# Kernel optimization log

Measured on AMD Instinct MI355X. Metric: run time of the kernel, lower is better.

## Reference

```python
import jax, jax.numpy as jnp
import numpy as np

PROCESSING_SPEED = 8.0  # init kwarg: softmax temperature
EPS = 1e-8              # torch F.cosine_similarity eps
BATCH, SIZE, DIM = 1024, 65536, 512


def setup_inputs() -> dict:
    key = jax.random.key(0)
    k1, k2 = jax.random.split(key)
    x = jax.random.normal(k1, (BATCH, DIM), dtype=jnp.float32)
    memory_bank = jax.random.normal(k2, (SIZE, DIM), dtype=jnp.float32)
    return {"x": x, "memory_bank": memory_bank}


def reference(x, memory_bank):
    # Cosine similarity between every query and every memory row, computed as
    # normalized dot products (math-equivalent to F.cosine_similarity with
    # denominator clamp max(||a||*||b||, eps), avoiding the (B,S,D) broadcast).
    x_norm = jnp.linalg.norm(x, axis=1, keepdims=True)            # (B, 1)
    m_norm = jnp.linalg.norm(memory_bank, axis=1, keepdims=True)  # (S, 1)
    dots = jnp.einsum('bd,sd->bs', x, memory_bank)                # (B, S)
    sims = dots / jnp.maximum(x_norm * m_norm.T, EPS)             # (B, S)
    attention = jax.nn.softmax(sims * PROCESSING_SPEED, axis=1)   # (B, S)
    return attention @ memory_bank                                # (B, D)
```

## Files before the change

kernel.cpp:

```cpp
#include <hip/hip_runtime.h>
#include <hip/hip_bf16.h>
#include <stdint.h>

#define B_N 1024
#define S_N 65536
#define D_N 512
#define NS 32
#define SC (S_N / NS)
#define SB 256
#define NSUB (SC / SB)

typedef __attribute__((ext_vector_type(8))) short bf16x8;
typedef __attribute__((ext_vector_type(4))) float f32x4;
typedef __attribute__((ext_vector_type(16))) float f32x16;

#define OFF_MBF   ((size_t)0)
#define OFF_MT    (OFF_MBF + (size_t)S_N * D_N * 2)
#define OFF_XBF   (OFF_MT  + (size_t)D_N * S_N * 2)
#define OFF_RX    (OFF_XBF + (size_t)B_N * D_N * 2)
#define OFF_RM    (OFF_RX  + (size_t)B_N * 4)
#define OFF_LSUM  (OFF_RM  + (size_t)S_N * 4)
#define OFF_OPART (OFF_LSUM + (size_t)B_N * 4)

__device__ __forceinline__ unsigned short f2bf(float f) {
  unsigned u = __builtin_bit_cast(unsigned, f);
  u += 0x7fffu + ((u >> 16) & 1u);
  return (unsigned short)(u >> 16);
}

__device__ __forceinline__ void stage16(const unsigned short* g, unsigned short* l) {
  __builtin_amdgcn_global_load_lds(
      (const __attribute__((address_space(1))) void*)g,
      (__attribute__((address_space(3))) void*)l, 16, 0, 0);
}

__global__ void k_prep_x(const float* __restrict__ X, unsigned short* __restrict__ Xbf,
                         float* __restrict__ rx) {
  const int row = blockIdx.x;
  const int t = threadIdx.x;
  float4 v = ((const float4*)(X + (size_t)row * D_N))[t];
  float ss = v.x*v.x + v.y*v.y + v.z*v.z + v.w*v.w;
  ushort4 o; o.x = f2bf(v.x); o.y = f2bf(v.y); o.z = f2bf(v.z); o.w = f2bf(v.w);
  ((ushort4*)(Xbf + (size_t)row * D_N))[t] = o;
  #pragma unroll
  for (int m = 1; m < 64; m <<= 1) ss += __shfl_xor(ss, m);
  __shared__ float partial[2];
  if ((t & 63) == 0) partial[t >> 6] = ss;
  __syncthreads();
  if (t == 0) rx[row] = 11.541560327111707f * rsqrtf(fmaxf(partial[0] + partial[1], 1e-24f));
}

__global__ void k_prep_m(const float* __restrict__ M, unsigned short* __restrict__ Mbf,
                         unsigned short* __restrict__ Mt, float* __restrict__ rm) {
  __shared__ float ts[64 * 65];
  const int t = threadIdx.x;
  const int s0 = blockIdx.x * 64;
  const int r = t >> 2, cq = t & 3;
  const int c = t >> 2, sq = t & 3;
  float ss = 0.f;
  for (int ct = 0; ct < 8; ++ct) {
    float f[16];
    const float4* src = (const float4*)(M + (size_t)(s0 + r) * D_N + ct * 64 + cq * 16);
    #pragma unroll
    for (int k = 0; k < 4; ++k) {
      float4 v = src[k];
      f[4*k+0] = v.x; f[4*k+1] = v.y; f[4*k+2] = v.z; f[4*k+3] = v.w;
    }
    union { unsigned short u[16]; uint4 v4[2]; } pk;
    #pragma unroll
    for (int j = 0; j < 16; ++j) {
      ss += f[j] * f[j];
      pk.u[j] = f2bf(f[j]);
      ts[r * 65 + cq * 16 + j] = f[j];
    }
    uint4* dst = (uint4*)(Mbf + (size_t)(s0 + r) * D_N + ct * 64 + cq * 16);
    dst[0] = pk.v4[0]; dst[1] = pk.v4[1];
    __syncthreads();
    union { unsigned short u[16]; uint4 v4[2]; } pt;
    #pragma unroll
    for (int j = 0; j < 16; ++j) pt.u[j] = f2bf(ts[(sq * 16 + j) * 65 + c]);
    uint4* dt = (uint4*)(Mt + (size_t)(ct * 64 + c) * S_N + s0 + sq * 16);
    dt[0] = pt.v4[0]; dt[1] = pt.v4[1];
    __syncthreads();
  }
  ss += __shfl_xor(ss, 1);
  ss += __shfl_xor(ss, 2);
  if (cq == 0) rm[s0 + r] = rsqrtf(fmaxf(ss, 1e-24f));
}

__global__ __launch_bounds__(512, 2) void k_fused(
    const unsigned short* __restrict__ Xbf, const unsigned short* __restrict__ Mbf,
    const unsigned short* __restrict__ Mt, const float* __restrict__ rx,
    const float* __restrict__ rminv, float* __restrict__ lsum,
    float* __restrict__ Opart) {
  __shared__ unsigned short Stg[2][24576];
  __shared__ unsigned short Ps[32768];

  const int t = threadIdx.x;
  const int w = t >> 6, lane = t & 63, l31 = lane & 31, hi = lane >> 5;
  const int qs = w >> 1, qcb = w & 1;
  const int hb = w >> 2, qd = w & 3;
  const int r7 = (l31 >> 1) & 7;
  const int p7 = l31 & 7;
  const int t3 = l31 & 3;
  const int sub8 = (lane & 1) * 8;
  const int rp15 = l31 >> 1;

  const int bid = blockIdx.x;
  const int xcd = bid & 7, slot = bid >> 3;
  const int bblk = slot & 7;
  const int chunk = xcd * 4 + (slot >> 3);
  const int b0 = bblk * 128;
  const int s0 = chunk * SC;

  const int mrow_t = ((t >> 4) << 1) | (t & 1);
  const int mc8    = ((((t >> 1) & 7) ^ ((t >> 4) & 7)) << 3);
  const int trow_t = t >> 2;
  const int tc8    = (((t & 3) ^ ((t >> 2) & 3)) << 3);

  #define ISS_QK(sS_, k0_, bi_) do {                                           \
    _Pragma("unroll")                                                          \
    for (int is = 0; is < 4; ++is)                                             \
      stage16(Mbf + (size_t)((sS_) + is * 64 + mrow_t) * D_N + (k0_) + mc8,    \
              &Stg[bi_][is * 4096 + w * 512]);                                 \
    _Pragma("unroll")                                                          \
    for (int is = 0; is < 2; ++is)                                             \
      stage16(Xbf + (size_t)(b0 + is * 64 + mrow_t) * D_N + (k0_) + mc8,       \
              &Stg[bi_][16384 + is * 4096 + w * 512]);                         \
  } while (0)
  #define ISS_T(sS_, ph_, bi_) do {                                            \
    _Pragma("unroll")                                                          \
    for (int is = 0; is < 4; ++is)                                             \
      stage16(Mt + (size_t)(is * 128 + trow_t) * S_N + (sS_) + (ph_) * 32 + tc8, \
              &Stg[bi_][is * 4096 + w * 512]);                                 \
  } while (0)

  f32x16 accO[2][4];
  #pragma unroll
  for (int i = 0; i < 2; ++i)
    #pragma unroll
    for (int j = 0; j < 4; ++j)
      #pragma unroll
      for (int r = 0; r < 16; ++r) accO[i][j][r] = 0.f;

  float ls[2] = {0.f, 0.f};
  float rxj[2];
  #pragma unroll
  for (int j = 0; j < 2; ++j) rxj[j] = rx[b0 + qcb * 64 + j * 32 + l31];

  ISS_QK(s0, 0, 0);

  for (int sub = 0; sub < NSUB; ++sub) {
    const int sS = s0 + sub * SB;

    f32x16 accP[2][2];
    #pragma unroll
    for (int i = 0; i < 2; ++i)
      #pragma unroll
      for (int j = 0; j < 2; ++j)
        #pragma unroll
        for (int r = 0; r < 16; ++r) accP[i][j][r] = 0.f;

    #pragma unroll
    for (int ph = 0; ph < 8; ++ph) {
      const int bi = ph & 1;
      if (ph < 7) { ISS_QK(sS, (ph + 1) * 64, bi ^ 1); }
      else        { ISS_T(sS, 0, bi ^ 1); }
      if (ph < 7) asm volatile("s_waitcnt vmcnt(6)" ::: "memory");
      else        asm volatile("s_waitcnt vmcnt(4)" ::: "memory");
      __builtin_amdgcn_s_barrier();
      const unsigned short* Ms = &Stg[bi][0];
      const unsigned short* Xs = &Stg[bi][16384];
      __builtin_amdgcn_s_setprio(1);
      #pragma unroll
      for (int ks = 0; ks < 4; ++ks) {
        const int c = ks * 2 + hi;
        bf16x8 aB[2], xB[2];
        #pragma unroll
        for (int i = 0; i < 2; ++i)
          aB[i] = *(const bf16x8*)&Ms[(qs * 32 + i * 16 + rp15) * 128 + ((c ^ r7) << 4) + sub8];
        #pragma unroll
        for (int j = 0; j < 2; ++j)
          xB[j] = *(const bf16x8*)&Xs[(qcb * 32 + j * 16 + rp15) * 128 + ((c ^ r7) << 4) + sub8];
        #pragma unroll
        for (int i = 0; i < 2; ++i)
          #pragma unroll
          for (int j = 0; j < 2; ++j)
            accP[i][j] = __builtin_amdgcn_mfma_f32_32x32x16_bf16(aB[i], xB[j], accP[i][j], 0, 0, 0);
      }
      __builtin_amdgcn_s_setprio(0);
      __builtin_amdgcn_s_barrier();
    }

    #pragma unroll
    for (int i = 0; i < 2; ++i)
      #pragma unroll
      for (int g = 0; g < 4; ++g) {
        const float4 rm = *(const float4*)&rminv[sS + qs * 64 + i * 32 + g * 8 + hi * 4];
        const int c16 = qs * 8 + i * 4 + g;
        #pragma unroll
        for (int j = 0; j < 2; ++j) {
          const float p0 = exp2f(accP[i][j][g * 4 + 0] * rxj[j] * rm.x);
          const float p1 = exp2f(accP[i][j][g * 4 + 1] * rxj[j] * rm.y);
          const float p2 = exp2f(accP[i][j][g * 4 + 2] * rxj[j] * rm.z);
          const float p3 = exp2f(accP[i][j][g * 4 + 3] * rxj[j] * rm.w);
          ls[j] += (p0 + p1) + (p2 + p3);
          const int brow = qcb * 64 + j * 32 + l31;
          uint2 pk;
          pk.x = (unsigned)f2bf(p0) | ((unsigned)f2bf(p1) << 16);
          pk.y = (unsigned)f2bf(p2) | ((unsigned)f2bf(p3) << 16);
          *(uint2*)&Ps[brow * 256 + ((c16 ^ p7) << 3) + hi * 4] = pk;
        }
      }
    asm volatile("s_waitcnt lgkmcnt(0)" ::: "memory");

    #pragma unroll
    for (int ph = 0; ph < 8; ++ph) {
      const int bi = ph & 1;
      if (ph < 7)                { ISS_T(sS, ph + 1, bi ^ 1); }
      else if (sub < NSUB - 1)   { ISS_QK(sS + SB, 0, bi ^ 1); }
      if (ph < 7)                     asm volatile("s_waitcnt vmcnt(4)" ::: "memory");
      else if (sub < NSUB - 1)        asm volatile("s_waitcnt vmcnt(6)" ::: "memory");
      else                            asm volatile("s_waitcnt vmcnt(0)" ::: "memory");
      __builtin_amdgcn_s_barrier();
      const unsigned short* Ts = &Stg[bi][0];
      __builtin_amdgcn_s_setprio(1);
      #pragma unroll
      for (int ks = 0; ks < 2; ++ks) {
        const int cP = ph * 4 + ks * 2 + hi;
        const int cT = ks * 2 + hi;
        bf16x8 pa[2], mB[4];
        #pragma unroll
        for (int i = 0; i < 2; ++i)
          pa[i] = *(const bf16x8*)&Ps[(hb * 64 + i * 32 + l31) * 256 + ((cP ^ p7) << 3)];
        #pragma unroll
        for (int j = 0; j < 4; ++j)
          mB[j] = *(const bf16x8*)&Ts[(qd * 128 + j * 32 + l31) * 32 + ((cT ^ t3) << 3)];
        #pragma unroll
        for (int i = 0; i < 2; ++i)
          #pragma unroll
          for (int j = 0; j < 4; ++j)
            accO[i][j] = __builtin_amdgcn_mfma_f32_32x32x16_bf16(pa[i], mB[j], accO[i][j], 0, 0, 0);
      }
      __builtin_amdgcn_s_setprio(0);
      __builtin_amdgcn_s_barrier();
    }
  }

  float* Od = Opart + (size_t)chunk * ((size_t)B_N * D_N);
  #pragma unroll
  for (int i = 0; i < 2; ++i)
    #pragma unroll
    for (int g = 0; g < 4; ++g)
      #pragma unroll
      for (int r = 0; r < 4; ++r) {
        const int bb = b0 + hb * 64 + i * 32 + g * 8 + hi * 4 + r;
        #pragma unroll
        for (int j = 0; j < 4; ++j) {
          const int d = qd * 128 + j * 32 + l31;
          Od[(size_t)bb * D_N + d] = accO[i][j][g * 4 + r];
        }
      }

  __syncthreads();
  float* red = (float*)&Stg[0][0];
  #pragma unroll
  for (int j = 0; j < 2; ++j) {
    float v = ls[j];
    v += __shfl_xor(v, 32);
    if (lane < 32) red[w * 64 + j * 32 + l31] = v;
  }
  __syncthreads();
  if (t < 128) {
    const int qc2 = t >> 6, idx = t & 63;
    float s = red[(0 + qc2) * 64 + idx] + red[(2 + qc2) * 64 + idx] +
              red[(4 + qc2) * 64 + idx] + red[(6 + qc2) * 64 + idx];
    unsafeAtomicAdd(&lsum[b0 + t], s);
  }
  #undef ISS_QK
  #undef ISS_T
}

__global__ void k_combine(const float* __restrict__ Opart, const float* __restrict__ lsum,
                          float* __restrict__ out) {
  const int idx = blockIdx.x * 256 + threadIdx.x;
  const int b = idx >> 7;
  float4 s = {0.f, 0.f, 0.f, 0.f};
  #pragma unroll
  for (int ks = 0; ks < NS; ++ks) {
    float4 v = ((const float4*)Opart)[(size_t)ks * (B_N * D_N / 4) + idx];
    s.x += v.x; s.y += v.y; s.z += v.z; s.w += v.w;
  }
  const float inv = 1.0f / lsum[b];
  s.x *= inv; s.y *= inv; s.z *= inv; s.w *= inv;
  ((float4*)out)[idx] = s;
}

extern "C" void kernel_launch(void* const* d_in, const int* in_sizes, int n_in,
                              void* d_out, int out_size, void* d_ws, size_t ws_size,
                              hipStream_t stream) {
  const float* X = (const float*)d_in[0];
  const float* M = (const float*)d_in[1];
  char* ws = (char*)d_ws;
  unsigned short* Mbf = (unsigned short*)(ws + OFF_MBF);
  unsigned short* Mt  = (unsigned short*)(ws + OFF_MT);
  unsigned short* Xbf = (unsigned short*)(ws + OFF_XBF);
  float* rxv  = (float*)(ws + OFF_RX);
  float* rmv  = (float*)(ws + OFF_RM);
  float* lsum = (float*)(ws + OFF_LSUM);
  float* Opart = (float*)(ws + OFF_OPART);

  hipMemsetAsync(lsum, 0, B_N * sizeof(float), stream);
  k_prep_x<<<dim3(B_N), 128, 0, stream>>>(X, Xbf, rxv);
  k_prep_m<<<dim3(S_N / 64), 256, 0, stream>>>(M, Mbf, Mt, rmv);
  k_fused<<<dim3(8 * NS), 512, 0, stream>>>(Xbf, Mbf, Mt, rxv, rmv, lsum, Opart);
  k_combine<<<dim3(B_N * D_N / 4 / 256), 256, 0, stream>>>(Opart, lsum, (float*)d_out);
}
```

Before: 489.3 us.

## Restage shared tiles as 64-wide swizzled rows and retile PV over d-halves

Staging of M, X and the transposed M now uses one layout, 64-element rows with an XOR-8 swizzle, in place of the earlier paired-row 128-wide and 32-wide layouts. Global loads now read 128-byte contiguous segments per row. The PV phase is retiled: each phase covers 64 s-columns of one d-half and does four k-steps with two B fragments, where before it covered 32 s-columns of all d with two k-steps. The output column mapping is adjusted to match. The aim is more coalesced global access and fewer LDS bank conflicts, at the cost of a different fragment reuse pattern.

New measurement: 481.8 us. Within noise of the previous version (-1.5%).

```diff
diff --git a/kernel.cpp b/kernel.cpp
--- a/kernel.cpp
+++ b/kernel.cpp
@@ -100,11 +100,7 @@
   const int w = t >> 6, lane = t & 63, l31 = lane & 31, hi = lane >> 5;
   const int qs = w >> 1, qcb = w & 1;
   const int hb = w >> 2, qd = w & 3;
-  const int r7 = (l31 >> 1) & 7;
   const int p7 = l31 & 7;
-  const int t3 = l31 & 3;
-  const int sub8 = (lane & 1) * 8;
-  const int rp15 = l31 >> 1;
 
   const int bid = blockIdx.x;
   const int xcd = bid & 7, slot = bid >> 3;
@@ -113,25 +109,24 @@
   const int b0 = bblk * 128;
   const int s0 = chunk * SC;
 
-  const int mrow_t = ((t >> 4) << 1) | (t & 1);
-  const int mc8    = ((((t >> 1) & 7) ^ ((t >> 4) & 7)) << 3);
-  const int trow_t = t >> 2;
-  const int tc8    = (((t & 3) ^ ((t >> 2) & 3)) << 3);
+  const int srow = t >> 3;
+  const int sch8 = ((t & 7) ^ (srow & 7)) * 8;
 
   #define ISS_QK(sS_, k0_, bi_) do {                                           \
     _Pragma("unroll")                                                          \
     for (int is = 0; is < 4; ++is)                                             \
-      stage16(Mbf + (size_t)((sS_) + is * 64 + mrow_t) * D_N + (k0_) + mc8,    \
+      stage16(Mbf + (size_t)((sS_) + is * 64 + srow) * D_N + (k0_) + sch8,     \
               &Stg[bi_][is * 4096 + w * 512]);                                 \
     _Pragma("unroll")                                                          \
     for (int is = 0; is < 2; ++is)                                             \
-      stage16(Xbf + (size_t)(b0 + is * 64 + mrow_t) * D_N + (k0_) + mc8,       \
+      stage16(Xbf + (size_t)(b0 + is * 64 + srow) * D_N + (k0_) + sch8,        \
               &Stg[bi_][16384 + is * 4096 + w * 512]);                         \
   } while (0)
   #define ISS_T(sS_, ph_, bi_) do {                                            \
     _Pragma("unroll")                                                          \
     for (int is = 0; is < 4; ++is)                                             \
-      stage16(Mt + (size_t)(is * 128 + trow_t) * S_N + (sS_) + (ph_) * 32 + tc8, \
+      stage16(Mt + (size_t)(((ph_) >> 2) * 256 + is * 64 + srow) * S_N         \
+                 + (sS_) + (((ph_) & 3) * 64) + sch8,                          \
               &Stg[bi_][is * 4096 + w * 512]);                                 \
   } while (0)
 
@@ -178,10 +173,10 @@
         bf16x8 aB[2], xB[2];
         #pragma unroll
         for (int i = 0; i < 2; ++i)
-          aB[i] = *(const bf16x8*)&Ms[(qs * 32 + i * 16 + rp15) * 128 + ((c ^ r7) << 4) + sub8];
+          aB[i] = *(const bf16x8*)&Ms[(qs * 64 + i * 32 + l31) * 64 + ((c ^ p7) << 3)];
         #pragma unroll
         for (int j = 0; j < 2; ++j)
-          xB[j] = *(const bf16x8*)&Xs[(qcb * 32 + j * 16 + rp15) * 128 + ((c ^ r7) << 4) + sub8];
+          xB[j] = *(const bf16x8*)&Xs[(qcb * 64 + j * 32 + l31) * 64 + ((c ^ p7) << 3)];
         #pragma unroll
         for (int i = 0; i < 2; ++i)
           #pragma unroll
@@ -224,23 +219,24 @@
       else                            asm volatile("s_waitcnt vmcnt(0)" ::: "memory");
       __builtin_amdgcn_s_barrier();
       const unsigned short* Ts = &Stg[bi][0];
+      const int dh = ph >> 2, sw = ph & 3;
       __builtin_amdgcn_s_setprio(1);
       #pragma unroll
-      for (int ks = 0; ks < 2; ++ks) {
-        const int cP = ph * 4 + ks * 2 + hi;
+      for (int ks = 0; ks < 4; ++ks) {
+        const int cP = sw * 8 + ks * 2 + hi;
         const int cT = ks * 2 + hi;
-        bf16x8 pa[2], mB[4];
+        bf16x8 pa[2], mB[2];
         #pragma unroll
         for (int i = 0; i < 2; ++i)
           pa[i] = *(const bf16x8*)&Ps[(hb * 64 + i * 32 + l31) * 256 + ((cP ^ p7) << 3)];
         #pragma unroll
-        for (int j = 0; j < 4; ++j)
-          mB[j] = *(const bf16x8*)&Ts[(qd * 128 + j * 32 + l31) * 32 + ((cT ^ t3) << 3)];
+        for (int jl = 0; jl < 2; ++jl)
+          mB[jl] = *(const bf16x8*)&Ts[(qd * 64 + jl * 32 + l31) * 64 + ((cT ^ p7) << 3)];
         #pragma unroll
         for (int i = 0; i < 2; ++i)
           #pragma unroll
-          for (int j = 0; j < 4; ++j)
-            accO[i][j] = __builtin_amdgcn_mfma_f32_32x32x16_bf16(pa[i], mB[j], accO[i][j], 0, 0, 0);
+          for (int jl = 0; jl < 2; ++jl)
+            accO[i][dh * 2 + jl] = __builtin_amdgcn_mfma_f32_32x32x16_bf16(pa[i], mB[jl], accO[i][dh * 2 + jl], 0, 0, 0);
       }
       __builtin_amdgcn_s_setprio(0);
       __builtin_amdgcn_s_barrier();
@@ -256,9 +252,9 @@
       for (int r = 0; r < 4; ++r) {
         const int bb = b0 + hb * 64 + i * 32 + g * 8 + hi * 4 + r;
         #pragma unroll
-        for (int j = 0; j < 4; ++j) {
-          const int d = qd * 128 + j * 32 + l31;
-          Od[(size_t)bb * D_N + d] = accO[i][j][g * 4 + r];
+        for (int jj = 0; jj < 4; ++jj) {
+          const int d = (jj >> 1) * 256 + qd * 64 + (jj & 1) * 32 + l31;
+          Od[(size_t)bb * D_N + d] = accO[i][jj][g * 4 + r];
         }
       }
 
```
